# Optimization experiments

Measured on AMD Instinct MI355X. Metric: run time of the kernel, lower is better.

## Reference

```python
import jax, jax.numpy as jnp
import numpy as np

SIGMA = 1.0


def setup_inputs() -> dict:
    key = jax.random.key(0)
    k1, k2 = jax.random.split(key)
    B, L = 32, 1024
    predictions = jax.random.normal(k1, (B, L), dtype=jnp.float32)
    targets = jax.random.randint(k2, (B, L), 0, 5).astype(jnp.float32)
    return {"predictions": predictions, "targets": targets}


def reference(predictions, targets):
    B, L = predictions.shape
    k = L  # self.k is None -> use full list
    # discounts[p] = 1/log2(p+2) for 0-based position p
    discounts = 1.0 / jnp.log2(jnp.arange(1, L + 1, dtype=jnp.float32) + 1.0)
    gains = 2.0 ** targets - 1.0  # [B, L]

    # rank[b, i] = 0-based position of item i when sorting pred descending
    order = jnp.argsort(-predictions, axis=1)
    rank = jnp.argsort(order, axis=1)
    # per-item discount; items ranked >= k contribute nothing to DCG@k
    disc_item = jnp.where(rank < k, discounts[rank], 0.0)  # [B, L]

    ideal_sorted = jnp.sort(gains, axis=1)[:, ::-1][:, :k]
    ideal_dcg = jnp.sum(ideal_sorted * discounts[:k], axis=1)  # [B]
    safe_ideal = jnp.where(ideal_dcg > 0, ideal_dcg, 1.0)

    gd = gains[:, :, None] - gains[:, None, :]        # [B, L, L]
    pd = predictions[:, :, None] - predictions[:, None, :]
    # active: gains differ and pair is misordered by predictions
    mask = ((gd > 0) & (pd < 0)) | ((gd < 0) & (pd > 0))

    # swapping items i,j only changes the two affected positions:
    # |delta_ndcg| = |g_i - g_j| * |disc_i - disc_j| / ideal_dcg
    delta_ndcg = (jnp.abs(gd)
                  * jnp.abs(disc_item[:, :, None] - disc_item[:, None, :])
                  / safe_ideal[:, None, None])
    sig = jax.nn.sigmoid(SIGMA * pd)
    rho = -SIGMA * delta_ndcg

    # per ordered pair (i,j): contribution to lambdas[i] and lambdas[j]
    c_first = jnp.where(mask, jnp.where(gd > 0, rho * (1.0 - sig), rho * sig), 0.0)
    c_second = jnp.where(mask, jnp.where(gd > 0, rho * sig, rho * (1.0 - sig)), 0.0)
    lambdas = c_first.sum(axis=2) + c_second.sum(axis=1)  # [B, L]

    pseudo = jnp.sum(predictions * lambdas, axis=1)  # [B]
    pseudo = jnp.where(ideal_dcg > 0, pseudo, 0.0)   # skip degenerate lists
    return jnp.sum(pseudo) / B
```

## Files before the change

kernel.cpp:

```cpp
#include <hip/hip_runtime.h>

constexpr int BATCH = 32;
constexpr int LEN   = 1024;

__device__ __forceinline__ unsigned key_of(float p) {
    unsigned u = __float_as_uint(p);
    return u ^ ((u & 0x80000000u) ? 0xFFFFFFFFu : 0x80000000u);
}

__global__ __launch_bounds__(256) void rank_kernel(
    const float* __restrict__ pred,
    const float* __restrict__ targ,
    float* __restrict__ disc_item,
    float* __restrict__ inv_ideal,
    float* __restrict__ out)
{
    __shared__ unsigned skey[LEN];
    __shared__ unsigned prank[256];
    __shared__ int      counts[8];
    __shared__ float    redbuf[4];

    const int blk  = blockIdx.x;
    const int b    = blk >> 4;
    const int iseg = blk & 15;
    const int t    = threadIdx.x;
    const bool do_ideal = (iseg == 0);

    if (t < 8) counts[t] = 0;
    if (blk == 0 && t == 0) out[0] = 0.0f;

    float4 pv = ((const float4*)(pred + b * LEN))[t];
    uint4 kv;
    kv.x = key_of(pv.x); kv.y = key_of(pv.y);
    kv.z = key_of(pv.z); kv.w = key_of(pv.w);
    ((uint4*)skey)[t] = kv;

    int myT[4];
    if (do_ideal) {
        float4 tv = ((const float4*)(targ + b * LEN))[t];
        myT[0] = (int)tv.x; myT[1] = (int)tv.y;
        myT[2] = (int)tv.z; myT[3] = (int)tv.w;
    }
    __syncthreads();

    if (do_ideal) {
        #pragma unroll
        for (int k = 0; k < 4; ++k) atomicAdd(&counts[myT[k]], 1);
    }

    const int jq   = t >> 6;
    const int lane = t & 63;
    const int i    = iseg * 64 + lane;
    const unsigned ki = skey[i];

    unsigned r = 0;
    const uint4* kq = (const uint4*)skey + jq * 64;
    #pragma unroll 8
    for (int c = 0; c < 64; ++c) {
        const uint4 k4 = kq[c];
        const int j0 = jq * 256 + c * 4;
        r += (k4.x > ki) || (k4.x == ki && (j0 + 0) < i);
        r += (k4.y > ki) || (k4.y == ki && (j0 + 1) < i);
        r += (k4.z > ki) || (k4.z == ki && (j0 + 2) < i);
        r += (k4.w > ki) || (k4.w == ki && (j0 + 3) < i);
    }
    prank[t] = r;
    __syncthreads();

    if (t < 64) {
        const unsigned rank = prank[t] + prank[t + 64] + prank[t + 128] + prank[t + 192];
        disc_item[b * LEN + iseg * 64 + t] = 1.0f / log2f((float)(rank + 2));
    }

    if (do_ideal) {
        const int c15 = counts[4];
        const int c7  = c15 + counts[3];
        const int c3  = c7  + counts[2];
        const int c1  = c3  + counts[1];
        float partial = 0.0f;
        #pragma unroll
        for (int k = 0; k < 4; ++k) {
            const int p = t + k * 256;
            const float g = (p < c15) ? 15.f : (p < c7) ? 7.f : (p < c3) ? 3.f
                           : (p < c1) ? 1.f : 0.f;
            partial += g / log2f((float)(p + 2));
        }
        for (int off = 32; off; off >>= 1) partial += __shfl_down(partial, off);
        if ((t & 63) == 0) redbuf[t >> 6] = partial;
        __syncthreads();
        if (t == 0) {
            const float ideal = redbuf[0] + redbuf[1] + redbuf[2] + redbuf[3];
            inv_ideal[b] = (ideal > 0.0f) ? (1.0f / ideal) : 0.0f;
        }
    }
}

__global__ __launch_bounds__(256) void pair_kernel(
    const float* __restrict__ pred,
    const float* __restrict__ targ,
    const float* __restrict__ disc_item,
    const float* __restrict__ inv_ideal,
    float* __restrict__ out)
{
    __shared__ float sg[LEN];
    __shared__ float sd[LEN];
    __shared__ float redbuf[4];

    const int blk  = blockIdx.x;
    const int b    = blk >> 4;
    const int jseg = blk & 15;
    const int t    = threadIdx.x;

    {
        float4 t4 = ((const float4*)(targ + b * LEN))[t];
        float4 g4;
        g4.x = (float)((1 << (int)t4.x) - 1);
        g4.y = (float)((1 << (int)t4.y) - 1);
        g4.z = (float)((1 << (int)t4.z) - 1);
        g4.w = (float)((1 << (int)t4.w) - 1);
        ((float4*)sg)[t] = g4;
        float4 d4 = ((const float4*)(disc_item + b * LEN))[t];
        ((float4*)sd)[t] = d4;
    }
    const float4 pi = ((const float4*)(pred + b * LEN))[t];
    __syncthreads();

    const float4 gi = ((const float4*)sg)[t];
    const float4 di = ((const float4*)sd)[t];

    float a0 = 0.f, a1 = 0.f, a2 = 0.f, a3 = 0.f;
    const int cbase = jseg * 16;
    #pragma unroll 4
    for (int c = 0; c < 16; ++c) {
        const float4 gj4 = ((const float4*)sg)[cbase + c];
        const float4 dj4 = ((const float4*)sd)[cbase + c];
        const float gjv[4] = {gj4.x, gj4.y, gj4.z, gj4.w};
        const float djv[4] = {dj4.x, dj4.y, dj4.z, dj4.w};
        #pragma unroll
        for (int u = 0; u < 4; ++u) {
            const float gj = gjv[u], dj = djv[u];
            a0 += fminf((gi.x - gj) * (di.x - dj), 0.f);
            a1 += fminf((gi.y - gj) * (di.y - dj), 0.f);
            a2 += fminf((gi.z - gj) * (di.z - dj), 0.f);
            a3 += fminf((gi.w - gj) * (di.w - dj), 0.f);
        }
    }

    float part = a0 * pi.x + a1 * pi.y + a2 * pi.z + a3 * pi.w;
    for (int off = 32; off; off >>= 1) part += __shfl_down(part, off);
    if ((t & 63) == 0) redbuf[t >> 6] = part;
    __syncthreads();
    if (t == 0) {
        const float s = (redbuf[0] + redbuf[1] + redbuf[2] + redbuf[3])
                        * inv_ideal[b] * (1.0f / (float)BATCH);
        atomicAdd(out, s);
    }
}

extern "C" void kernel_launch(void* const* d_in, const int* in_sizes, int n_in,
                              void* d_out, int out_size, void* d_ws, size_t ws_size,
                              hipStream_t stream) {
    const float* pred = (const float*)d_in[0];
    const float* targ = (const float*)d_in[1];
    float* out = (float*)d_out;
    float* disc_item = (float*)d_ws;
    float* inv_ideal = disc_item + BATCH * LEN;

    rank_kernel<<<BATCH * 16, 256, 0, stream>>>(pred, targ, disc_item, inv_ideal, out);
    pair_kernel<<<BATCH * 16, 256, 0, stream>>>(pred, targ, disc_item, inv_ideal, out);
}
```

Before: 73.64 us.

## Fuse rank and pair kernels into one cooperative launch with grid sync

Merges the rank/ideal-DCG kernel and the pairwise lambda kernel into a single cooperative kernel separated by a grid-wide barrier. Predictions and gains stay in registers and shared memory across both phases instead of being reloaded, and one kernel launch is removed. The cost is a grid sync, the cooperative-launch requirement that all 512 blocks be co-resident, and higher shared-memory use per block. Only the per-row discounts still go through global memory.

```diff
diff --git a/kernel.cpp b/kernel.cpp
--- a/kernel.cpp
+++ b/kernel.cpp
@@ -1,4 +1,7 @@
 #include <hip/hip_runtime.h>
+#include <hip/hip_cooperative_groups.h>
+
+namespace cg = cooperative_groups;
 
 constexpr int BATCH = 32;
 constexpr int LEN   = 1024;
@@ -8,7 +11,7 @@
     return u ^ ((u & 0x80000000u) ? 0xFFFFFFFFu : 0x80000000u);
 }
 
-__global__ __launch_bounds__(256) void rank_kernel(
+__global__ __launch_bounds__(256) void fused_kernel(
     const float* __restrict__ pred,
     const float* __restrict__ targ,
     float* __restrict__ disc_item,
@@ -19,38 +22,43 @@
     __shared__ unsigned prank[256];
     __shared__ int      counts[8];
     __shared__ float    redbuf[4];
+    __shared__ float    sg[LEN];
+    __shared__ float    sd[LEN];
 
-    const int blk  = blockIdx.x;
-    const int b    = blk >> 4;
-    const int iseg = blk & 15;
-    const int t    = threadIdx.x;
-    const bool do_ideal = (iseg == 0);
+    const int blk = blockIdx.x;
+    const int b   = blk >> 4;
+    const int seg = blk & 15;
+    const int t   = threadIdx.x;
+    const bool do_ideal = (seg == 0);
 
+    if (blk == 0 && t == 0) atomicExch(out, 0.0f);
     if (t < 8) counts[t] = 0;
-    if (blk == 0 && t == 0) out[0] = 0.0f;
 
-    float4 pv = ((const float4*)(pred + b * LEN))[t];
+    const float4 pv = ((const float4*)(pred + b * LEN))[t];
     uint4 kv;
     kv.x = key_of(pv.x); kv.y = key_of(pv.y);
     kv.z = key_of(pv.z); kv.w = key_of(pv.w);
     ((uint4*)skey)[t] = kv;
 
-    int myT[4];
-    if (do_ideal) {
-        float4 tv = ((const float4*)(targ + b * LEN))[t];
-        myT[0] = (int)tv.x; myT[1] = (int)tv.y;
-        myT[2] = (int)tv.z; myT[3] = (int)tv.w;
-    }
+    const float4 tv = ((const float4*)(targ + b * LEN))[t];
+    float4 g4;
+    g4.x = (float)((1 << (int)tv.x) - 1);
+    g4.y = (float)((1 << (int)tv.y) - 1);
+    g4.z = (float)((1 << (int)tv.z) - 1);
+    g4.w = (float)((1 << (int)tv.w) - 1);
+    ((float4*)sg)[t] = g4;
     __syncthreads();
 
     if (do_ideal) {
-        #pragma unroll
-        for (int k = 0; k < 4; ++k) atomicAdd(&counts[myT[k]], 1);
+        atomicAdd(&counts[(int)tv.x], 1);
+        atomicAdd(&counts[(int)tv.y], 1);
+        atomicAdd(&counts[(int)tv.z], 1);
+        atomicAdd(&counts[(int)tv.w], 1);
     }
 
     const int jq   = t >> 6;
     const int lane = t & 63;
-    const int i    = iseg * 64 + lane;
+    const int i    = seg * 64 + lane;
     const unsigned ki = skey[i];
 
     unsigned r = 0;
@@ -69,7 +77,7 @@
 
     if (t < 64) {
         const unsigned rank = prank[t] + prank[t + 64] + prank[t + 128] + prank[t + 192];
-        disc_item[b * LEN + iseg * 64 + t] = 1.0f / log2f((float)(rank + 2));
+        disc_item[b * LEN + seg * 64 + t] = 1.0f / log2f((float)(rank + 2));
     }
 
     if (do_ideal) {
@@ -93,43 +101,19 @@
             inv_ideal[b] = (ideal > 0.0f) ? (1.0f / ideal) : 0.0f;
         }
     }
-}
 
-__global__ __launch_bounds__(256) void pair_kernel(
-    const float* __restrict__ pred,
-    const float* __restrict__ targ,
-    const float* __restrict__ disc_item,
-    const float* __restrict__ inv_ideal,
-    float* __restrict__ out)
-{
-    __shared__ float sg[LEN];
-    __shared__ float sd[LEN];
-    __shared__ float redbuf[4];
+    cg::this_grid().sync();
 
-    const int blk  = blockIdx.x;
-    const int b    = blk >> 4;
-    const int jseg = blk & 15;
-    const int t    = threadIdx.x;
-
-    {
-        float4 t4 = ((const float4*)(targ + b * LEN))[t];
-        float4 g4;
-        g4.x = (float)((1 << (int)t4.x) - 1);
-        g4.y = (float)((1 << (int)t4.y) - 1);
-        g4.z = (float)((1 << (int)t4.z) - 1);
-        g4.w = (float)((1 << (int)t4.w) - 1);
-        ((float4*)sg)[t] = g4;
-        float4 d4 = ((const float4*)(disc_item + b * LEN))[t];
-        ((float4*)sd)[t] = d4;
-    }
-    const float4 pi = ((const float4*)(pred + b * LEN))[t];
+    const float4 d4 = ((const float4*)(disc_item + b * LEN))[t];
+    ((float4*)sd)[t] = d4;
     __syncthreads();
 
-    const float4 gi = ((const float4*)sg)[t];
-    const float4 di = ((const float4*)sd)[t];
+    const float4 pi = pv;
+    const float4 gi = g4;
+    const float4 di = d4;
 
     float a0 = 0.f, a1 = 0.f, a2 = 0.f, a3 = 0.f;
-    const int cbase = jseg * 16;
+    const int cbase = seg * 16;
     #pragma unroll 4
     for (int c = 0; c < 16; ++c) {
         const float4 gj4 = ((const float4*)sg)[cbase + c];
@@ -166,6 +150,9 @@
     float* disc_item = (float*)d_ws;
     float* inv_ideal = disc_item + BATCH * LEN;
 
-    rank_kernel<<<BATCH * 16, 256, 0, stream>>>(pred, targ, disc_item, inv_ideal, out);
-    pair_kernel<<<BATCH * 16, 256, 0, stream>>>(pred, targ, disc_item, inv_ideal, out);
+    void* args[] = { (void*)&pred, (void*)&targ, (void*)&disc_item,
+                     (void*)&inv_ideal, (void*)&out };
+    hipLaunchCooperativeKernel((const void*)fused_kernel,
+                               dim3(BATCH * 16), dim3(256),
+                               args, 0, stream);
 }
```

After: 129.9 us. +76.4%, slower.
